# Kernel optimization log

Measured on AMD Instinct MI355X. Metric: run time of the kernel, lower is better.

Reference implementation:

```python
import jax, jax.numpy as jnp
import numpy as np

N = 4096     # batch of positions
E = 32       # descriptor buckets (experts)
NBLK = 12    # residual blocks per head


def _ln(x, g, b, eps=1e-5):
    m = x.mean(-1, keepdims=True)
    v = ((x - m) ** 2).mean(-1, keepdims=True)
    return (x - m) / jnp.sqrt(v + eps) * g + b


def _gelu(x):
    return jax.nn.gelu(x, approximate=False)  # torch nn.GELU default = exact erf


def setup_inputs() -> dict:
    key = jax.random.key(0)
    ks = iter(jax.random.split(key, 64))

    def nrm(shape, scale=0.05):
        return jax.random.normal(next(ks), shape, jnp.float32) * scale

    return {
        "piece_idx": jax.random.randint(next(ks), (N, 64), 0, 12),
        "side_flag": jax.random.randint(next(ks), (N,), 0, 2),
        "ep_file": jax.random.randint(next(ks), (N,), 0, 8),
        "castle_ms": jax.random.uniform(next(ks), (N, 4), jnp.float32),
        "fifty_a": jax.random.uniform(next(ks), (N,), jnp.float32),
        "descriptor_index": jax.random.randint(next(ks), (N,), 0, E),
        # per-bucket embedding tables, stacked on a leading expert axis
        "Wp_w": nrm((E, 64, 12, 32)), "Wp_b": nrm((E, 64, 12, 32)),
        "Wc_w": nrm((E, 4, 32)), "Wc_b": nrm((E, 4, 32)),
        "Wep_w": nrm((E, 8, 32)), "Wep_b": nrm((E, 8, 32)),
        "Wf_w": nrm((E, 2, 32)), "Wf_b": nrm((E, 2, 32)),
        # per-bucket MLP head params (weights stored as [in,out])
        "fc1_w": nrm((E, 2240, 256)), "fc1_b": nrm((E, 256)),
        "ln1_g": jnp.ones((E, 256)), "ln1_b": jnp.zeros((E, 256)),
        "fc2_w": nrm((E, 256, 32)), "fc2_b": nrm((E, 32)),
        "ln2_g": jnp.ones((E, 32)), "ln2_b": jnp.zeros((E, 32)),
        "blkA_w": nrm((NBLK, E, 32, 32)), "blkA_b": nrm((NBLK, E, 32)),
        "blkA_g": jnp.ones((NBLK, E, 32)), "blkA_be": jnp.zeros((NBLK, E, 32)),
        "blkB_w": nrm((NBLK, E, 32, 32)), "blkB_b": nrm((NBLK, E, 32)),
        "blkB_g": jnp.ones((NBLK, E, 32)), "blkB_be": jnp.zeros((NBLK, E, 32)),
        "out_w": nrm((E, 32, 51)), "out_b": nrm((E, 51)),
        "bins": jnp.linspace(0.0, 1.0, 51),
    }


def reference(piece_idx, side_flag, ep_file, castle_ms, fifty_a, descriptor_index,
              Wp_w, Wp_b, Wc_w, Wc_b, Wep_w, Wep_b, Wf_w, Wf_b,
              fc1_w, fc1_b, ln1_g, ln1_b, fc2_w, fc2_b, ln2_g, ln2_b,
              blkA_w, blkA_b, blkA_g, blkA_be, blkB_w, blkB_b, blkB_g, blkB_be,
              out_w, out_b, bins):
    desc = descriptor_index
    side = side_flag.astype(bool)
    n = piece_idx.shape[0]

    # ---- per-bucket, side-selected embedding gathers -> x_emb [N,2240] ----
    sq = jnp.arange(64)
    pc = jnp.maximum(piece_idx, 0)                                 # clamp -1 -> 0
    w_emb = Wp_w[desc[:, None], sq[None, :], pc]                    # [N,64,32]
    b_emb = Wp_b[desc[:, None], sq[None, :], pc]
    piece_emb = jnp.where(side[:, None, None], b_emb, w_emb)
    piece_emb = piece_emb * (piece_idx >= 0)[..., None].astype(piece_emb.dtype)
    pieces_vec = piece_emb.reshape(n, 2048)

    Wc = jnp.where(side[:, None, None], Wc_b[desc], Wc_w[desc])     # [N,4,32]
    castle_vec = (castle_ms[..., None] * Wc).reshape(n, 128)

    Wep = jnp.where(side[:, None, None], Wep_b[desc], Wep_w[desc])  # [N,8,32]
    epc = jnp.maximum(ep_file, 0)
    ep_vec = jnp.take_along_axis(Wep, epc[:, None, None], axis=1)[:, 0]
    ep_vec = ep_vec * (ep_file >= 0)[:, None].astype(ep_vec.dtype)

    Wf = jnp.where(side[:, None, None], Wf_b[desc], Wf_w[desc])     # [N,2,32]
    fifty_vec = (1.0 - fifty_a)[:, None] * Wf[:, 0] + fifty_a[:, None] * Wf[:, 1]

    x = jnp.concatenate([pieces_vec, castle_vec, ep_vec, fifty_vec], axis=1)  # [N,2240]

    # ---- expert-routed dense layer: all-expert GEMM + per-token select ----
    def dense_moe(h, W, b):
        ha = jnp.einsum('nd,edh->neh', h, W)                        # [N,E,out]
        hsel = jnp.take_along_axis(ha, desc[:, None, None], axis=1)[:, 0]
        return hsel + b[desc]

    h = _ln(_gelu(dense_moe(x, fc1_w, fc1_b)), ln1_g[desc], ln1_b[desc])   # [N,256]
    h = _ln(_gelu(dense_moe(h, fc2_w, fc2_b)), ln2_g[desc], ln2_b[desc])   # [N,32]

    def blk(carry, p):
        wA, bA, gA, beA, wB, bB, gB, beB = p
        y = _ln(_gelu(dense_moe(carry, wA, bA)), gA[desc], beA[desc])
        y = _ln(_gelu(dense_moe(y, wB, bB)), gB[desc], beB[desc])
        return carry + y, None

    h, _ = jax.lax.scan(blk, h, (blkA_w, blkA_b, blkA_g, blkA_be,
                                 blkB_w, blkB_b, blkB_g, blkB_be))

    logits = dense_moe(_gelu(h), out_w, out_b)                      # [N,51]
    p_win = jnp.sum(jax.nn.softmax(logits, axis=-1) * bins, axis=-1, keepdims=True)
    return logits, p_win
```

## Files before the change

### kernel.cpp

```cpp
#include <hip/hip_runtime.h>
#include <math.h>

#define N 4096
#define E 32
#define NBLK 12
#define D_IN 2240
#define H1 256
#define H2 32
#define NOUT 51
#define MT 16
#define NPAD (N + E*(MT-1))
#define NTILE (NPAD/MT)
#define KSPLIT 4
#define NROWS 4608
#define GMAX 96
#define NCONVBLK (35*4*E)

typedef short s8v __attribute__((ext_vector_type(8)));
typedef float f4v __attribute__((ext_vector_type(4)));

__device__ __forceinline__ float gelu(float x){
    return 0.5f * x * (1.0f + erff(x * 0.70710678118654752f));
}
__device__ __forceinline__ unsigned short f2bf(float f){
    unsigned int u = __float_as_uint(f);
    unsigned int r = (u + 0x7fffu + ((u >> 16) & 1u)) >> 16;
    return (unsigned short)r;
}
__device__ __forceinline__ float bflo(unsigned int u){ return __uint_as_float(u << 16); }
__device__ __forceinline__ float bfhi(unsigned int u){ return __uint_as_float(u & 0xffff0000u); }

template<int CTRL>
__device__ __forceinline__ float dppadd(float x){
    int y = __builtin_amdgcn_update_dpp(0, __float_as_int(x), CTRL, 0xF, 0xF, true);
    return x + __int_as_float(y);
}
__device__ __forceinline__ float red32(float x){
    x = dppadd<0x121>(x);
    x = dppadd<0x122>(x);
    x = dppadd<0x124>(x);
    x = dppadd<0x128>(x);
    int y = __builtin_amdgcn_ds_swizzle(__float_as_int(x), 0x401F);
    return x + __int_as_float(y);
}

__global__ void k_sort(const int* __restrict__ desc,
                       int* __restrict__ perm, int* __restrict__ tile_e,
                       int4* __restrict__ garr, int* __restrict__ ngroups){
    __shared__ int scnt[E];
    __shared__ int spoff[E+1];
    __shared__ int scur[E];
    int tid = threadIdx.x;
    if (tid < E) scnt[tid] = 0;
    __syncthreads();
    for (int n = tid; n < N; n += blockDim.x) atomicAdd(&scnt[desc[n]], 1);
    __syncthreads();
    if (tid == 0){
        int run = 0;
        for (int e = 0; e < E; e++){ spoff[e] = run; run += ((scnt[e] + MT - 1)/MT)*MT; }
        spoff[E] = run;
        int ng = 0;
        for (int e = 0; e < E; e++){
            int t0 = spoff[e]/MT, t1 = spoff[e+1]/MT;
            for (int t = t0; t < t1; t += 8){
                int nv = t1 - t; if (nv > 8) nv = 8;
                if (ng < GMAX) garr[ng] = make_int4(t, e, nv, 0);
                ng++;
            }
        }
        *ngroups = (ng > GMAX) ? GMAX : ng;
    }
    __syncthreads();
    if (tid < E) scur[tid] = spoff[tid];
    for (int p = tid; p < NPAD; p += blockDim.x) perm[p] = -1;
    __syncthreads();
    for (int n = tid; n < N; n += blockDim.x){
        int p = atomicAdd(&scur[desc[n]], 1);
        perm[p] = n;
    }
    for (int t = tid; t < NTILE; t += blockDim.x){
        int p0 = t*MT;
        int e = -1;
        if (p0 < spoff[E]){
            for (int q = 0; q < E; q++){
                if (p0 >= spoff[q] && p0 < spoff[q+1]){ e = q; break; }
            }
        }
        tile_e[t] = e;
    }
}

__global__ void k_prep(const int* __restrict__ perm,
                       const int* __restrict__ piece_idx,
                       const int* __restrict__ side_flag,
                       const int* __restrict__ ep_file,
                       const float* __restrict__ castle_ms,
                       const float* __restrict__ fifty_a,
                       const int* __restrict__ desc_idx,
                       const float* __restrict__ Wp_w, const float* __restrict__ Wp_b,
                       const float* __restrict__ Wc_w, const float* __restrict__ Wc_b,
                       const float* __restrict__ Wep_w, const float* __restrict__ Wep_b,
                       const float* __restrict__ Wf_w, const float* __restrict__ Wf_b,
                       unsigned short* __restrict__ xs,
                       const float* __restrict__ W1, unsigned short* __restrict__ Wt){
    __shared__ float lds[64][65];
    int tid = threadIdx.x;
    if (blockIdx.x >= NPAD){
        int b = blockIdx.x - NPAD;
        int kt = b % 35;
        int nt = (b / 35) & 3;
        int e  = b / 140;
        int k0 = kt*64, n0 = nt*64;
        int kk = tid >> 4, nn = (tid & 15) * 4;
        const float* src = W1 + ((size_t)e*D_IN + k0)*H1 + n0;
        #pragma unroll
        for (int r = 0; r < 4; r++){
            float4 v = *(const float4*)(src + (size_t)(kk + r*16)*H1 + nn);
            lds[kk + r*16][nn]   = v.x;
            lds[kk + r*16][nn+1] = v.y;
            lds[kk + r*16][nn+2] = v.z;
            lds[kk + r*16][nn+3] = v.w;
        }
        __syncthreads();
        int n = tid >> 2, kq = tid & 3;
        s8v p0, p1;
        #pragma unroll
        for (int j = 0; j < 8; j++) p0[j] = (short)f2bf(lds[kq*16 + j][n]);
        #pragma unroll
        for (int j = 0; j < 8; j++) p1[j] = (short)f2bf(lds[kq*16 + 8 + j][n]);
        unsigned short* dst = Wt + ((size_t)(e*H1 + n0 + n))*D_IN + k0 + kq*16;
        *(s8v*)dst       = p0;
        *(s8v*)(dst + 8) = p1;
        return;
    }
    int pos = blockIdx.x;
    int row = perm[pos];
    unsigned short* xr = xs + (size_t)pos * D_IN;
    if (row < 0){
        s8v z = {0,0,0,0,0,0,0,0};
        for (int t = tid; t < D_IN/8; t += blockDim.x) *(s8v*)(xr + t*8) = z;
        return;
    }
    int d = desc_idx[row];
    int s = side_flag[row];
    __shared__ int pidx[64];
    if (tid < 64) pidx[tid] = piece_idx[row*64 + tid];
    __syncthreads();
    const float* Wp  = s ? Wp_b  : Wp_w;
    const float* Wc  = s ? Wc_b  : Wc_w;
    const float* Wep = s ? Wep_b : Wep_w;
    const float* Wf  = s ? Wf_b  : Wf_w;
    int ep  = ep_file[row];
    int epc = ep > 0 ? ep : 0;
    float a = fifty_a[row];
    for (int t = tid; t < D_IN/8; t += blockDim.x){
        int i0 = t*8;
        float v[8];
        if (i0 < 2048){
            int sq = i0 >> 5, c0 = i0 & 31;
            int pc = pidx[sq];
            float msk = pc >= 0 ? 1.0f : 0.0f;
            int pcc = pc > 0 ? pc : 0;
            const float* base = Wp + (((size_t)d*64 + sq)*12 + pcc)*32 + c0;
            float4 a0 = *(const float4*)base;
            float4 a1 = *(const float4*)(base + 4);
            v[0]=a0.x*msk; v[1]=a0.y*msk; v[2]=a0.z*msk; v[3]=a0.w*msk;
            v[4]=a1.x*msk; v[5]=a1.y*msk; v[6]=a1.z*msk; v[7]=a1.w*msk;
        } else if (i0 < 2176){
            int j = i0 - 2048; int ci = j >> 5, c0 = j & 31;
            float cv = castle_ms[row*4 + ci];
            const float* base = Wc + ((size_t)d*4 + ci)*32 + c0;
            float4 a0 = *(const float4*)base;
            float4 a1 = *(const float4*)(base + 4);
            v[0]=a0.x*cv; v[1]=a0.y*cv; v[2]=a0.z*cv; v[3]=a0.w*cv;
            v[4]=a1.x*cv; v[5]=a1.y*cv; v[6]=a1.z*cv; v[7]=a1.w*cv;
        } else if (i0 < 2208){
            int c0 = i0 - 2176;
            float msk = ep >= 0 ? 1.0f : 0.0f;
            const float* base = Wep + ((size_t)d*8 + epc)*32 + c0;
            float4 a0 = *(const float4*)base;
            float4 a1 = *(const float4*)(base + 4);
            v[0]=a0.x*msk; v[1]=a0.y*msk; v[2]=a0.z*msk; v[3]=a0.w*msk;
            v[4]=a1.x*msk; v[5]=a1.y*msk; v[6]=a1.z*msk; v[7]=a1.w*msk;
        } else {
            int c0 = i0 - 2208;
            #pragma unroll
            for (int j = 0; j < 8; j++)
                v[j] = (1.0f - a) * Wf[(size_t)d*64 + c0 + j] + a * Wf[(size_t)d*64 + 32 + c0 + j];
        }
        s8v p;
        #pragma unroll
        for (int j = 0; j < 8; j++) p[j] = (short)f2bf(v[j]);
        *(s8v*)(xr + i0) = p;
    }
}

__launch_bounds__(256)
__global__ void k_fc1(const int4* __restrict__ garr, const int* __restrict__ ngroups,
                      const unsigned short* __restrict__ xs,
                      const unsigned short* __restrict__ Wt,
                      float* __restrict__ h1p){
    int g = blockIdx.x;
    if (g >= *ngroups) return;
    int4 gi = garr[g];
    int tile0 = gi.x, e = gi.y, nv = gi.z;
    int kc = blockIdx.y, nh = blockIdx.z;
    int kstart = (kc <= 2) ? kc*18 : 53;
    int nsteps = (kc < 2) ? 18 : 17;
    int lane = threadIdx.x & 63, wave = threadIdx.x >> 6;
    int quad = lane >> 4, l16 = lane & 15;
    int col0 = nh*128 + wave*32 + l16;
    const unsigned short* Ab = xs + (size_t)(tile0*MT + l16)*D_IN + quad*8;
    const unsigned short* B0 = Wt + ((size_t)e*H1 + col0)*D_IN + quad*8;
    const unsigned short* B1 = B0 + (size_t)16*D_IN;
    f4v acc[8][2];
    #pragma unroll
    for (int mt = 0; mt < 8; mt++){ acc[mt][0] = (f4v){0.f,0.f,0.f,0.f}; acc[mt][1] = (f4v){0.f,0.f,0.f,0.f}; }
    int kend = kstart + nsteps;
    #pragma unroll 2
    for (int s = kstart; s < kend; s++){
        int ko = s*32;
        s8v b0 = *(const s8v*)(B0 + ko);
        s8v b1 = *(const s8v*)(B1 + ko);
        #pragma unroll
        for (int mt = 0; mt < 8; mt++){
            s8v av = *(const s8v*)(Ab + (size_t)mt*MT*D_IN + ko);
            acc[mt][0] = __builtin_amdgcn_mfma_f32_16x16x32_bf16(av, b0, acc[mt][0], 0, 0, 0);
            acc[mt][1] = __builtin_amdgcn_mfma_f32_16x16x32_bf16(av, b1, acc[mt][1], 0, 0, 0);
        }
    }
    float* out = h1p + (size_t)kc*NROWS*H1;
    #pragma unroll
    for (int mt = 0; mt < 8; mt++){
        if (mt >= nv) break;
        int posb = (tile0 + mt)*MT + quad*4;
        #pragma unroll
        for (int r = 0; r < 4; r++){
            out[(size_t)(posb + r)*H1 + col0]      = acc[mt][0][r];
            out[(size_t)(posb + r)*H1 + col0 + 16] = acc[mt][1][r];
        }
    }
}

__launch_bounds__(512)
__global__ void k_tail(const int* __restrict__ tile_e, const int* __restrict__ perm,
                       const float* __restrict__ h1p, const float* __restrict__ b1,
                       const float* __restrict__ g1, const float* __restrict__ be1,
                       const float* __restrict__ W2, const float* __restrict__ b2,
                       const float* __restrict__ g2, const float* __restrict__ be2,
                       const float* __restrict__ Aw, const float* __restrict__ Abv,
                       const float* __restrict__ Ag, const float* __restrict__ Abe,
                       const float* __restrict__ Bw, const float* __restrict__ Bb,
                       const float* __restrict__ Bg, const float* __restrict__ Bbe,
                       const float* __restrict__ Ow, const float* __restrict__ Ob,
                       const float* __restrict__ bins,
                       float* __restrict__ out){
    int t = blockIdx.x;
    int e = tile_e[t];
    if (e < 0) return;
    int tid = threadIdx.x;

    __shared__ __align__(16) unsigned int smem[12288];
    __shared__ __align__(16) float vecs[NBLK*6*32];
    __shared__ __align__(16) float sh2[MT][36];
    __shared__ __align__(16) float sh3[MT][36];

    float* shf = (float*)smem;
    unsigned int* W2pk = smem + 4160;

    unsigned int wreg[24];
    {
        int h = tid & 1, q = tid >> 1, cc = q & 31, p2 = q >> 5;
        int k0 = 4*p2 + 2*h;
        #pragma unroll
        for (int i = 0; i < 24; i++){
            const float* src = (i & 1) ? Bw : Aw;
            size_t base = ((size_t)(i >> 1)*E + e)*1024;
            unsigned int lo = f2bf(src[base + k0*32 + cc]);
            unsigned int hi = f2bf(src[base + (k0+1)*32 + cc]);
            wreg[i] = lo | (hi << 16);
        }
    }
    {
        const float* W2e = W2 + (size_t)e*H1*H2;
        for (int j = tid; j < 4096; j += 512){
            int h = j & 1, q = j >> 1, cc = q & 31, p2 = q >> 5;
            int k0 = 4*p2 + 2*h;
            unsigned int lo = f2bf(W2e[k0*32 + cc]);
            unsigned int hi = f2bf(W2e[(k0+1)*32 + cc]);
            W2pk[(p2*32 + cc)*2 + h] = lo | (hi << 16);
        }
    }
    for (int j = tid; j < NBLK*6*32; j += 512){
        int cc = j & 31, vi = (j >> 5) % 6, tb = j / 192;
        size_t wb = (size_t)tb*E + e;
        const float* src;
        switch(vi){ case 0: src=Abv; break; case 1: src=Ag; break; case 2: src=Abe; break;
                    case 3: src=Bb;  break; case 4: src=Bg; break; default: src=Bbe; }
        vecs[j] = src[wb*32 + cc];
    }
    for (int slot = tid; slot < MT*64; slot += 512){
        int r = slot >> 6, c4 = (slot & 63) << 2;
        int row = t*MT + r;
        float4 v = {0.f,0.f,0.f,0.f};
        #pragma unroll
        for (int kc = 0; kc < KSPLIT; kc++){
            float4 p = *(const float4*)(h1p + ((size_t)kc*NROWS + row)*H1 + c4);
            v.x += p.x; v.y += p.y; v.z += p.z; v.w += p.w;
        }
        float4 bb = *(const float4*)(b1 + e*H1 + c4);
        shf[r*260 + c4]   = gelu(v.x + bb.x);
        shf[r*260 + c4+1] = gelu(v.y + bb.y);
        shf[r*260 + c4+2] = gelu(v.z + bb.z);
        shf[r*260 + c4+3] = gelu(v.w + bb.w);
    }
    __syncthreads();

    int m = tid >> 5, c = tid & 31;
    {
        float s = 0.f, s2 = 0.f;
        #pragma unroll
        for (int j = 0; j < 8; j++){
            float x = shf[m*260 + c + 32*j];
            s += x; s2 += x*x;
        }
        s  = red32(s);
        s2 = red32(s2);
        float mean = s * (1.0f/H1);
        float var  = s2 * (1.0f/H1) - mean*mean;
        float rs = rsqrtf(var + 1e-5f);
        #pragma unroll
        for (int j = 0; j < 8; j++){
            int k = c + 32*j;
            shf[m*260 + k] = (shf[m*260 + k] - mean) * rs * g1[e*H1 + k] + be1[e*H1 + k];
        }
    }
    float hv;
    {
        const uint2* W2p = (const uint2*)W2pk;
        float q0=0.f,q1=0.f,q2=0.f,q3=0.f;
        #pragma unroll 8
        for (int p2 = 0; p2 < 64; p2++){
            uint2 w = W2p[p2*32 + c];
            float4 h4 = *(const float4*)(shf + m*260 + p2*4);
            q0 = fmaf(h4.x, bflo(w.x), q0);
            q1 = fmaf(h4.y, bfhi(w.x), q1);
            q2 = fmaf(h4.z, bflo(w.y), q2);
            q3 = fmaf(h4.w, bfhi(w.y), q3);
        }
        float acc = (q0+q1) + (q2+q3) + b2[e*H2 + c];
        float y = gelu(acc);
        float s  = red32(y);
        float s2 = red32(y*y);
        float mean2 = s * (1.0f/H2);
        float var2  = s2 * (1.0f/H2) - mean2*mean2;
        hv = (y - mean2) * rsqrtf(var2 + 1e-5f) * g2[e*H2+c] + be2[e*H2+c];
    }
    __syncthreads();

    #pragma unroll
    for (int i = 0; i < 24; i++) smem[i*512 + tid] = wreg[i];
    __syncthreads();

    for (int tb = 0; tb < NBLK; tb++){
        const float* vA = &vecs[tb*192];
        const uint2* WA = (const uint2*)(smem + (tb*2+0)*512);
        const uint2* WB = (const uint2*)(smem + (tb*2+1)*512);
        sh2[m][c] = hv;
        float q0=0.f,q1=0.f,q2=0.f,q3=0.f;
        #pragma unroll
        for (int p2 = 0; p2 < 8; p2++){
            uint2 w = WA[p2*32 + c];
            float4 h4 = *(const float4*)(&sh2[m][p2*4]);
            q0 = fmaf(h4.x, bflo(w.x), q0);
            q1 = fmaf(h4.y, bfhi(w.x), q1);
            q2 = fmaf(h4.z, bflo(w.y), q2);
            q3 = fmaf(h4.w, bfhi(w.y), q3);
        }
        float ya = (q0+q1) + (q2+q3) + vA[c];
        ya = gelu(ya);
        float sa  = red32(ya);
        float sa2 = red32(ya*ya);
        float ma = sa * (1.0f/H2);
        float va = sa2 * (1.0f/H2) - ma*ma;
        float yA = (ya - ma) * rsqrtf(va + 1e-5f) * vA[32+c] + vA[64+c];
        sh3[m][c] = yA;
        q0=0.f; q1=0.f; q2=0.f; q3=0.f;
        #pragma unroll
        for (int p2 = 0; p2 < 8; p2++){
            uint2 w = WB[p2*32 + c];
            float4 h4 = *(const float4*)(&sh3[m][p2*4]);
            q0 = fmaf(h4.x, bflo(w.x), q0);
            q1 = fmaf(h4.y, bfhi(w.x), q1);
            q2 = fmaf(h4.z, bflo(w.y), q2);
            q3 = fmaf(h4.w, bfhi(w.y), q3);
        }
        float yb = (q0+q1) + (q2+q3) + vA[96+c];
        yb = gelu(yb);
        float sb  = red32(yb);
        float sb2 = red32(yb*yb);
        float mb = sb * (1.0f/H2);
        float vb = sb2 * (1.0f/H2) - mb*mb;
        hv += (yb - mb) * rsqrtf(vb + 1e-5f) * vA[128+c] + vA[160+c];
    }

    sh2[m][c] = gelu(hv);
    __syncthreads();
    int wave = tid >> 6, lane = tid & 63;
    const float* W = Ow + (size_t)e*32*NOUT;
    for (int rr = wave; rr < MT; rr += 8){
        int orow = perm[t*MT + rr];
        if (orow < 0) continue;
        float acc = (lane < NOUT) ? Ob[e*NOUT + lane] : -INFINITY;
        #pragma unroll
        for (int k = 0; k < 32; k++){
            float gk = sh2[rr][k];
            if (lane < NOUT) acc = fmaf(gk, W[k*NOUT + lane], acc);
        }
        if (lane < NOUT) out[(size_t)orow*NOUT + lane] = acc;
        float mx = acc;
        #pragma unroll
        for (int o = 32; o > 0; o >>= 1) mx = fmaxf(mx, __shfl_xor(mx, o));
        float pp = (lane < NOUT) ? expf(acc - mx) : 0.0f;
        float sum = pp;
        float pb = (lane < NOUT) ? pp * bins[lane] : 0.0f;
        float sb = pb;
        #pragma unroll
        for (int o = 32; o > 0; o >>= 1){ sum += __shfl_xor(sum, o); sb += __shfl_xor(sb, o); }
        if (lane == 0) out[(size_t)N*NOUT + orow] = sb / sum;
    }
}

extern "C" void kernel_launch(void* const* d_in, const int* in_sizes, int n_in,
                              void* d_out, int out_size, void* d_ws, size_t ws_size,
                              hipStream_t stream){
    const int*   piece_idx = (const int*)d_in[0];
    const int*   side_flag = (const int*)d_in[1];
    const int*   ep_file   = (const int*)d_in[2];
    const float* castle_ms = (const float*)d_in[3];
    const float* fifty_a   = (const float*)d_in[4];
    const int*   desc      = (const int*)d_in[5];
    const float* Wp_w  = (const float*)d_in[6];
    const float* Wp_b  = (const float*)d_in[7];
    const float* Wc_w  = (const float*)d_in[8];
    const float* Wc_b  = (const float*)d_in[9];
    const float* Wep_w = (const float*)d_in[10];
    const float* Wep_b = (const float*)d_in[11];
    const float* Wf_w  = (const float*)d_in[12];
    const float* Wf_b  = (const float*)d_in[13];
    const float* fc1_w = (const float*)d_in[14];
    const float* fc1_b = (const float*)d_in[15];
    const float* ln1_g = (const float*)d_in[16];
    const float* ln1_b = (const float*)d_in[17];
    const float* fc2_w = (const float*)d_in[18];
    const float* fc2_b = (const float*)d_in[19];
    const float* ln2_g = (const float*)d_in[20];
    const float* ln2_b = (const float*)d_in[21];
    const float* blkA_w  = (const float*)d_in[22];
    const float* blkA_b  = (const float*)d_in[23];
    const float* blkA_g  = (const float*)d_in[24];
    const float* blkA_be = (const float*)d_in[25];
    const float* blkB_w  = (const float*)d_in[26];
    const float* blkB_b  = (const float*)d_in[27];
    const float* blkB_g  = (const float*)d_in[28];
    const float* blkB_be = (const float*)d_in[29];
    const float* out_w = (const float*)d_in[30];
    const float* out_b = (const float*)d_in[31];
    const float* bins  = (const float*)d_in[32];

    char* wsp = (char*)d_ws;
    auto alloc = [&](size_t bytes){ void* p = (void*)wsp; wsp += (bytes + 255) & ~(size_t)255; return p; };
    int*            perm    = (int*)            alloc((size_t)NPAD*4);
    int*            tile_e  = (int*)            alloc((size_t)NTILE*4);
    int4*           garr    = (int4*)           alloc((size_t)GMAX*16);
    int*            ngroups = (int*)            alloc(256);
    unsigned short* Wt      = (unsigned short*) alloc((size_t)E*H1*D_IN*2);
    unsigned short* xs      = (unsigned short*) alloc((size_t)(NPAD+128)*D_IN*2);
    float*          h1p     = (float*)          alloc((size_t)KSPLIT*NROWS*H1*4);

    k_sort<<<1, 256, 0, stream>>>(desc, perm, tile_e, garr, ngroups);
    k_prep<<<NPAD + NCONVBLK, 256, 0, stream>>>(perm, piece_idx, side_flag, ep_file,
                                                castle_ms, fifty_a, desc,
                                                Wp_w, Wp_b, Wc_w, Wc_b,
                                                Wep_w, Wep_b, Wf_w, Wf_b,
                                                xs, fc1_w, Wt);
    k_fc1<<<dim3(GMAX, KSPLIT, 2), 256, 0, stream>>>(garr, ngroups, xs, Wt, h1p);
    k_tail<<<NTILE, 512, 0, stream>>>(tile_e, perm, h1p, fc1_b, ln1_g, ln1_b,
                                      fc2_w, fc2_b, ln2_g, ln2_b,
                                      blkA_w, blkA_b, blkA_g, blkA_be,
                                      blkB_w, blkB_b, blkB_g, blkB_be,
                                      out_w, out_b, bins, (float*)d_out);
}
```

Baseline: 312.0 us.

## Double k_tail block to 1024 threads, splitting each row's dot-products across two half-waves

Result: no change. 310.3 us (-0.5%).

```diff
diff --git a/kernel.cpp b/kernel.cpp
--- a/kernel.cpp
+++ b/kernel.cpp
@@ -242,7 +242,7 @@
     }
 }
 
-__launch_bounds__(512)
+__launch_bounds__(1024, 8)
 __global__ void k_tail(const int* __restrict__ tile_e, const int* __restrict__ perm,
                        const float* __restrict__ h1p, const float* __restrict__ b1,
                        const float* __restrict__ g1, const float* __restrict__ be1,
@@ -268,14 +268,17 @@
     float* shf = (float*)smem;
     unsigned int* W2pk = smem + 4160;
 
-    unsigned int wreg[24];
+    unsigned int wreg[12];
     {
-        int h = tid & 1, q = tid >> 1, cc = q & 31, p2 = q >> 5;
-        int k0 = 4*p2 + 2*h;
-        #pragma unroll
-        for (int i = 0; i < 24; i++){
-            const float* src = (i & 1) ? Bw : Aw;
-            size_t base = ((size_t)(i >> 1)*E + e)*1024;
+        #pragma unroll
+        for (int i = 0; i < 12; i++){
+            int f = i*1024 + tid;
+            int mi = f >> 9;
+            int slot = f & 511;
+            int h = slot & 1, q = slot >> 1, cc = q & 31, p2 = q >> 5;
+            int k0 = 4*p2 + 2*h;
+            const float* src = (mi & 1) ? Bw : Aw;
+            size_t base = ((size_t)(mi >> 1)*E + e)*1024;
             unsigned int lo = f2bf(src[base + k0*32 + cc]);
             unsigned int hi = f2bf(src[base + (k0+1)*32 + cc]);
             wreg[i] = lo | (hi << 16);
@@ -283,7 +286,7 @@
     }
     {
         const float* W2e = W2 + (size_t)e*H1*H2;
-        for (int j = tid; j < 4096; j += 512){
+        for (int j = tid; j < 4096; j += 1024){
             int h = j & 1, q = j >> 1, cc = q & 31, p2 = q >> 5;
             int k0 = 4*p2 + 2*h;
             unsigned int lo = f2bf(W2e[k0*32 + cc]);
@@ -291,7 +294,7 @@
             W2pk[(p2*32 + cc)*2 + h] = lo | (hi << 16);
         }
     }
-    for (int j = tid; j < NBLK*6*32; j += 512){
+    for (int j = tid; j < NBLK*6*32; j += 1024){
         int cc = j & 31, vi = (j >> 5) % 6, tb = j / 192;
         size_t wb = (size_t)tb*E + e;
         const float* src;
@@ -299,7 +302,8 @@
                     case 3: src=Bb;  break; case 4: src=Bg; break; default: src=Bbe; }
         vecs[j] = src[wb*32 + cc];
     }
-    for (int slot = tid; slot < MT*64; slot += 512){
+    {
+        int slot = tid;
         int r = slot >> 6, c4 = (slot & 63) << 2;
         int row = t*MT + r;
         float4 v = {0.f,0.f,0.f,0.f};
@@ -316,22 +320,26 @@
     }
     __syncthreads();
 
-    int m = tid >> 5, c = tid & 31;
+    int m = tid >> 6;
+    int lane = tid & 63;
+    int c = lane & 31;
+    int half = lane >> 5;
+
     {
         float s = 0.f, s2 = 0.f;
         #pragma unroll
-        for (int j = 0; j < 8; j++){
-            float x = shf[m*260 + c + 32*j];
+        for (int j = 0; j < 4; j++){
+            float x = shf[m*260 + lane + 64*j];
             s += x; s2 += x*x;
         }
-        s  = red32(s);
-        s2 = red32(s2);
+        s  = red32(s);  s  += __shfl_xor(s, 32);
+        s2 = red32(s2); s2 += __shfl_xor(s2, 32);
         float mean = s * (1.0f/H1);
         float var  = s2 * (1.0f/H1) - mean*mean;
         float rs = rsqrtf(var + 1e-5f);
         #pragma unroll
-        for (int j = 0; j < 8; j++){
-            int k = c + 32*j;
+        for (int j = 0; j < 4; j++){
+            int k = lane + 64*j;
             shf[m*260 + k] = (shf[m*260 + k] - mean) * rs * g1[e*H1 + k] + be1[e*H1 + k];
         }
     }
@@ -339,8 +347,10 @@
     {
         const uint2* W2p = (const uint2*)W2pk;
         float q0=0.f,q1=0.f,q2=0.f,q3=0.f;
+        int p2b = half*32;
         #pragma unroll 8
-        for (int p2 = 0; p2 < 64; p2++){
+        for (int p2i = 0; p2i < 32; p2i++){
+            int p2 = p2b + p2i;
             uint2 w = W2p[p2*32 + c];
             float4 h4 = *(const float4*)(shf + m*260 + p2*4);
             q0 = fmaf(h4.x, bflo(w.x), q0);
@@ -348,7 +358,9 @@
             q2 = fmaf(h4.z, bflo(w.y), q2);
             q3 = fmaf(h4.w, bfhi(w.y), q3);
         }
-        float acc = (q0+q1) + (q2+q3) + b2[e*H2 + c];
+        float acc = (q0+q1) + (q2+q3);
+        acc += __shfl_xor(acc, 32);
+        acc += b2[e*H2 + c];
         float y = gelu(acc);
         float s  = red32(y);
         float s2 = red32(y*y);
@@ -359,17 +371,19 @@
     __syncthreads();
 
     #pragma unroll
-    for (int i = 0; i < 24; i++) smem[i*512 + tid] = wreg[i];
+    for (int i = 0; i < 12; i++) smem[i*1024 + tid] = wreg[i];
     __syncthreads();
 
     for (int tb = 0; tb < NBLK; tb++){
         const float* vA = &vecs[tb*192];
         const uint2* WA = (const uint2*)(smem + (tb*2+0)*512);
         const uint2* WB = (const uint2*)(smem + (tb*2+1)*512);
-        sh2[m][c] = hv;
+        if (half == 0) sh2[m][c] = hv;
         float q0=0.f,q1=0.f,q2=0.f,q3=0.f;
-        #pragma unroll
-        for (int p2 = 0; p2 < 8; p2++){
+        int p2b = half*4;
+        #pragma unroll
+        for (int p2i = 0; p2i < 4; p2i++){
+            int p2 = p2b + p2i;
             uint2 w = WA[p2*32 + c];
             float4 h4 = *(const float4*)(&sh2[m][p2*4]);
             q0 = fmaf(h4.x, bflo(w.x), q0);
@@ -377,17 +391,20 @@
             q2 = fmaf(h4.z, bflo(w.y), q2);
             q3 = fmaf(h4.w, bfhi(w.y), q3);
         }
-        float ya = (q0+q1) + (q2+q3) + vA[c];
+        float ya = (q0+q1) + (q2+q3);
+        ya += __shfl_xor(ya, 32);
+        ya += vA[c];
         ya = gelu(ya);
         float sa  = red32(ya);
         float sa2 = red32(ya*ya);
         float ma = sa * (1.0f/H2);
         float va = sa2 * (1.0f/H2) - ma*ma;
         float yA = (ya - ma) * rsqrtf(va + 1e-5f) * vA[32+c] + vA[64+c];
-        sh3[m][c] = yA;
+        if (half == 0) sh3[m][c] = yA;
         q0=0.f; q1=0.f; q2=0.f; q3=0.f;
         #pragma unroll
-        for (int p2 = 0; p2 < 8; p2++){
+        for (int p2i = 0; p2i < 4; p2i++){
+            int p2 = p2b + p2i;
             uint2 w = WB[p2*32 + c];
             float4 h4 = *(const float4*)(&sh3[m][p2*4]);
             q0 = fmaf(h4.x, bflo(w.x), q0);
@@ -395,7 +412,9 @@
             q2 = fmaf(h4.z, bflo(w.y), q2);
             q3 = fmaf(h4.w, bfhi(w.y), q3);
         }
-        float yb = (q0+q1) + (q2+q3) + vA[96+c];
+        float yb = (q0+q1) + (q2+q3);
+        yb += __shfl_xor(yb, 32);
+        yb += vA[96+c];
         yb = gelu(yb);
         float sb  = red32(yb);
         float sb2 = red32(yb*yb);
@@ -404,30 +423,32 @@
         hv += (yb - mb) * rsqrtf(vb + 1e-5f) * vA[128+c] + vA[160+c];
     }
 
-    sh2[m][c] = gelu(hv);
-    __syncthreads();
-    int wave = tid >> 6, lane = tid & 63;
+    if (half == 0) sh2[m][c] = gelu(hv);
+    __syncthreads();
+    int wave = tid >> 6;
     const float* W = Ow + (size_t)e*32*NOUT;
-    for (int rr = wave; rr < MT; rr += 8){
+    {
+        int rr = wave;
         int orow = perm[t*MT + rr];
-        if (orow < 0) continue;
-        float acc = (lane < NOUT) ? Ob[e*NOUT + lane] : -INFINITY;
-        #pragma unroll
-        for (int k = 0; k < 32; k++){
-            float gk = sh2[rr][k];
-            if (lane < NOUT) acc = fmaf(gk, W[k*NOUT + lane], acc);
-        }
-        if (lane < NOUT) out[(size_t)orow*NOUT + lane] = acc;
-        float mx = acc;
-        #pragma unroll
-        for (int o = 32; o > 0; o >>= 1) mx = fmaxf(mx, __shfl_xor(mx, o));
-        float pp = (lane < NOUT) ? expf(acc - mx) : 0.0f;
-        float sum = pp;
-        float pb = (lane < NOUT) ? pp * bins[lane] : 0.0f;
-        float sb = pb;
-        #pragma unroll
-        for (int o = 32; o > 0; o >>= 1){ sum += __shfl_xor(sum, o); sb += __shfl_xor(sb, o); }
-        if (lane == 0) out[(size_t)N*NOUT + orow] = sb / sum;
+        if (orow >= 0){
+            float acc = (lane < NOUT) ? Ob[e*NOUT + lane] : -INFINITY;
+            #pragma unroll
+            for (int k = 0; k < 32; k++){
+                float gk = sh2[rr][k];
+                if (lane < NOUT) acc = fmaf(gk, W[k*NOUT + lane], acc);
+            }
+            if (lane < NOUT) out[(size_t)orow*NOUT + lane] = acc;
+            float mx = acc;
+            #pragma unroll
+            for (int o = 32; o > 0; o >>= 1) mx = fmaxf(mx, __shfl_xor(mx, o));
+            float pp = (lane < NOUT) ? expf(acc - mx) : 0.0f;
+            float sum = pp;
+            float pb = (lane < NOUT) ? pp * bins[lane] : 0.0f;
+            float sb = pb;
+            #pragma unroll
+            for (int o = 32; o > 0; o >>= 1){ sum += __shfl_xor(sum, o); sb += __shfl_xor(sb, o); }
+            if (lane == 0) out[(size_t)N*NOUT + orow] = sb / sum;
+        }
     }
 }
 
@@ -485,9 +506,9 @@
                                                 Wep_w, Wep_b, Wf_w, Wf_b,
                                                 xs, fc1_w, Wt);
     k_fc1<<<dim3(GMAX, KSPLIT, 2), 256, 0, stream>>>(garr, ngroups, xs, Wt, h1p);
-    k_tail<<<NTILE, 512, 0, stream>>>(tile_e, perm, h1p, fc1_b, ln1_g, ln1_b,
-                                      fc2_w, fc2_b, ln2_g, ln2_b,
-                                      blkA_w, blkA_b, blkA_g, blkA_be,
-                                      blkB_w, blkB_b, blkB_g, blkB_be,
-                                      out_w, out_b, bins, (float*)d_out);
-}
+    k_tail<<<NTILE, 1024, 0, stream>>>(tile_e, perm, h1p, fc1_b, ln1_g, ln1_b,
+                                       fc2_w, fc2_b, ln2_g, ln2_b,
+                                       blkA_w, blkA_b, blkA_g, blkA_be,
+                                       blkB_w, blkB_b, blkB_g, blkB_be,
+                                       out_w, out_b, bins, (float*)d_out);
+}
```

## Split tail kernel into half-tiles and double-buffer residual block weights

Applied to the files above, without the earlier changes.

Measured after the change: 300.6 us. 1.04x faster.

```diff
diff --git a/kernel.cpp b/kernel.cpp
--- a/kernel.cpp
+++ b/kernel.cpp
@@ -242,7 +242,7 @@
     }
 }
 
-__launch_bounds__(512)
+__launch_bounds__(256)
 __global__ void k_tail(const int* __restrict__ tile_e, const int* __restrict__ perm,
                        const float* __restrict__ h1p, const float* __restrict__ b1,
                        const float* __restrict__ g1, const float* __restrict__ be1,
@@ -255,35 +255,23 @@
                        const float* __restrict__ Ow, const float* __restrict__ Ob,
                        const float* __restrict__ bins,
                        float* __restrict__ out){
-    int t = blockIdx.x;
+    int th = blockIdx.x;
+    int t  = th >> 1;
+    int r0 = (th & 1) * 8;
     int e = tile_e[t];
     if (e < 0) return;
     int tid = threadIdx.x;
 
-    __shared__ __align__(16) unsigned int smem[12288];
-    __shared__ __align__(16) float vecs[NBLK*6*32];
-    __shared__ __align__(16) float sh2[MT][36];
-    __shared__ __align__(16) float sh3[MT][36];
-
-    float* shf = (float*)smem;
-    unsigned int* W2pk = smem + 4160;
-
-    unsigned int wreg[24];
-    {
-        int h = tid & 1, q = tid >> 1, cc = q & 31, p2 = q >> 5;
-        int k0 = 4*p2 + 2*h;
-        #pragma unroll
-        for (int i = 0; i < 24; i++){
-            const float* src = (i & 1) ? Bw : Aw;
-            size_t base = ((size_t)(i >> 1)*E + e)*1024;
-            unsigned int lo = f2bf(src[base + k0*32 + cc]);
-            unsigned int hi = f2bf(src[base + (k0+1)*32 + cc]);
-            wreg[i] = lo | (hi << 16);
-        }
-    }
+    __shared__ __align__(16) float        shf[8*260];
+    __shared__ __align__(16) unsigned int W2pk[4096];
+    __shared__ __align__(16) float        vecs[NBLK*6*32];
+    __shared__ __align__(16) unsigned int wbuf[2][1024];
+    __shared__ __align__(16) float        sh2[8][36];
+    __shared__ __align__(16) float        sh3[8][36];
+
     {
         const float* W2e = W2 + (size_t)e*H1*H2;
-        for (int j = tid; j < 4096; j += 512){
+        for (int j = tid; j < 4096; j += 256){
             int h = j & 1, q = j >> 1, cc = q & 31, p2 = q >> 5;
             int k0 = 4*p2 + 2*h;
             unsigned int lo = f2bf(W2e[k0*32 + cc]);
@@ -291,7 +279,7 @@
             W2pk[(p2*32 + cc)*2 + h] = lo | (hi << 16);
         }
     }
-    for (int j = tid; j < NBLK*6*32; j += 512){
+    for (int j = tid; j < NBLK*6*32; j += 256){
         int cc = j & 31, vi = (j >> 5) % 6, tb = j / 192;
         size_t wb = (size_t)tb*E + e;
         const float* src;
@@ -299,9 +287,25 @@
                     case 3: src=Bb;  break; case 4: src=Bg; break; default: src=Bbe; }
         vecs[j] = src[wb*32 + cc];
     }
-    for (int slot = tid; slot < MT*64; slot += 512){
+    {
+        size_t base = (size_t)e*1024;
+        #pragma unroll
+        for (int k = 0; k < 4; k++){
+            int s_all = k*256 + tid;
+            int s = s_all & 511;
+            int h = s & 1, q = s >> 1, cc = q & 31, p2 = q >> 5;
+            int k0 = 4*p2 + 2*h;
+            const float* src = (s_all >> 9) ? Bw : Aw;
+            unsigned int lo = f2bf(src[base + k0*32 + cc]);
+            unsigned int hi = f2bf(src[base + (k0+1)*32 + cc]);
+            wbuf[0][s_all] = lo | (hi << 16);
+        }
+    }
+    #pragma unroll
+    for (int it = 0; it < 2; it++){
+        int slot = it*256 + tid;
         int r = slot >> 6, c4 = (slot & 63) << 2;
-        int row = t*MT + r;
+        int row = t*MT + r0 + r;
         float4 v = {0.f,0.f,0.f,0.f};
         #pragma unroll
         for (int kc = 0; kc < KSPLIT; kc++){
@@ -356,16 +360,27 @@
         float var2  = s2 * (1.0f/H2) - mean2*mean2;
         hv = (y - mean2) * rsqrtf(var2 + 1e-5f) * g2[e*H2+c] + be2[e*H2+c];
     }
-    __syncthreads();
-
-    #pragma unroll
-    for (int i = 0; i < 24; i++) smem[i*512 + tid] = wreg[i];
-    __syncthreads();
-
+
+    int cur = 0;
     for (int tb = 0; tb < NBLK; tb++){
+        float wfa[4], wfb[4];
+        int tbn = tb + 1;
+        if (tbn < NBLK){
+            size_t base = ((size_t)tbn*E + e)*1024;
+            #pragma unroll
+            for (int k = 0; k < 4; k++){
+                int s_all = k*256 + tid;
+                int s = s_all & 511;
+                int h = s & 1, q = s >> 1, cc = q & 31, p2 = q >> 5;
+                int k0 = 4*p2 + 2*h;
+                const float* src = (s_all >> 9) ? Bw : Aw;
+                wfa[k] = src[base + k0*32 + cc];
+                wfb[k] = src[base + (k0+1)*32 + cc];
+            }
+        }
         const float* vA = &vecs[tb*192];
-        const uint2* WA = (const uint2*)(smem + (tb*2+0)*512);
-        const uint2* WB = (const uint2*)(smem + (tb*2+1)*512);
+        const uint2* WA = (const uint2*)&wbuf[cur][0];
+        const uint2* WB = (const uint2*)&wbuf[cur][512];
         sh2[m][c] = hv;
         float q0=0.f,q1=0.f,q2=0.f,q3=0.f;
         #pragma unroll
@@ -402,14 +417,25 @@
         float mb = sb * (1.0f/H2);
         float vb = sb2 * (1.0f/H2) - mb*mb;
         hv += (yb - mb) * rsqrtf(vb + 1e-5f) * vA[128+c] + vA[160+c];
+        if (tbn < NBLK){
+            #pragma unroll
+            for (int k = 0; k < 4; k++){
+                int s_all = k*256 + tid;
+                unsigned int lo = f2bf(wfa[k]);
+                unsigned int hi = f2bf(wfb[k]);
+                wbuf[cur^1][s_all] = lo | (hi << 16);
+            }
+        }
+        cur ^= 1;
+        __syncthreads();
     }
 
     sh2[m][c] = gelu(hv);
     __syncthreads();
     int wave = tid >> 6, lane = tid & 63;
     const float* W = Ow + (size_t)e*32*NOUT;
-    for (int rr = wave; rr < MT; rr += 8){
-        int orow = perm[t*MT + rr];
+    for (int rr = wave; rr < 8; rr += 4){
+        int orow = perm[t*MT + r0 + rr];
         if (orow < 0) continue;
         float acc = (lane < NOUT) ? Ob[e*NOUT + lane] : -INFINITY;
         #pragma unroll
@@ -485,9 +511,9 @@
                                                 Wep_w, Wep_b, Wf_w, Wf_b,
                                                 xs, fc1_w, Wt);
     k_fc1<<<dim3(GMAX, KSPLIT, 2), 256, 0, stream>>>(garr, ngroups, xs, Wt, h1p);
-    k_tail<<<NTILE, 512, 0, stream>>>(tile_e, perm, h1p, fc1_b, ln1_g, ln1_b,
-                                      fc2_w, fc2_b, ln2_g, ln2_b,
-                                      blkA_w, blkA_b, blkA_g, blkA_be,
-                                      blkB_w, blkB_b, blkB_g, blkB_be,
-                                      out_w, out_b, bins, (float*)d_out);
-}
+    k_tail<<<NTILE*2, 256, 0, stream>>>(tile_e, perm, h1p, fc1_b, ln1_g, ln1_b,
+                                        fc2_w, fc2_b, ln2_g, ln2_b,
+                                        blkA_w, blkA_b, blkA_g, blkA_be,
+                                        blkB_w, blkB_b, blkB_g, blkB_be,
+                                        out_w, out_b, bins, (float*)d_out);
+}
```
